# Kernel tuning notes

Hardware: AMD Instinct MI355X
Metric: run time of the kernel (lower is better)

Reference implementation:

```python
import jax, jax.numpy as jnp
import numpy as np

N = 50000
E = 1600000
IN_DIM = 256
HID = 128
EPS = 1e-5


def _bn(x, gamma, beta):
    # BatchNorm1d forward in training mode: biased batch stats
    mean = jnp.mean(x, axis=0)
    var = jnp.mean((x - mean) ** 2, axis=0)
    return (x - mean) * jax.lax.rsqrt(var + EPS) * gamma + beta


def _sage(x, edge_index, Wl, bl, Wr):
    # PyG SAGEConv with mean aggregation:
    #   out = lin_l(mean_{j in N(i)} x_j) + lin_r(x_i)
    src, dst = edge_index[0], edge_index[1]
    agg = jax.ops.segment_sum(x[src], dst, num_segments=N)          # [N, H]
    cnt = jax.ops.segment_sum(jnp.ones((src.shape[0],), x.dtype), dst, num_segments=N)
    mean = agg / jnp.maximum(cnt, 1.0)[:, None]
    return mean @ Wl + bl + x @ Wr


def setup_inputs() -> dict:
    key = jax.random.key(0)
    ks = jax.random.split(key, 16)
    s_in = 1.0 / np.sqrt(IN_DIM)
    s_h = 1.0 / np.sqrt(HID)
    return {
        "x": jax.random.normal(ks[0], (N, IN_DIM), jnp.float32),
        "edge_index": jax.random.randint(ks[1], (2, E), 0, N, jnp.int32),
        # input_linear: Linear(IN_DIM, HID) + BN
        "W_in": jax.random.uniform(ks[2], (IN_DIM, HID), jnp.float32, -s_in, s_in),
        "b_in": jax.random.uniform(ks[3], (HID,), jnp.float32, -s_in, s_in),
        "g1": jnp.ones((HID,), jnp.float32), "be1": jnp.zeros((HID,), jnp.float32),
        # hidden_linear: Linear(HID, HID) + BN
        "W_hid": jax.random.uniform(ks[4], (HID, HID), jnp.float32, -s_h, s_h),
        "b_hid": jax.random.uniform(ks[5], (HID,), jnp.float32, -s_h, s_h),
        "g2": jnp.ones((HID,), jnp.float32), "be2": jnp.zeros((HID,), jnp.float32),
        # graph_conv1: SAGEConv(HID, HID) + BN
        "Wl1": jax.random.uniform(ks[6], (HID, HID), jnp.float32, -s_h, s_h),
        "bl1": jax.random.uniform(ks[7], (HID,), jnp.float32, -s_h, s_h),
        "Wr1": jax.random.uniform(ks[8], (HID, HID), jnp.float32, -s_h, s_h),
        "g3": jnp.ones((HID,), jnp.float32), "be3": jnp.zeros((HID,), jnp.float32),
        # graph_conv2: SAGEConv(HID, HID) + BN
        "Wl2": jax.random.uniform(ks[9], (HID, HID), jnp.float32, -s_h, s_h),
        "bl2": jax.random.uniform(ks[10], (HID,), jnp.float32, -s_h, s_h),
        "Wr2": jax.random.uniform(ks[11], (HID, HID), jnp.float32, -s_h, s_h),
        "g4": jnp.ones((HID,), jnp.float32), "be4": jnp.zeros((HID,), jnp.float32),
    }


def reference(x, edge_index, W_in, b_in, g1, be1, W_hid, b_hid, g2, be2,
              Wl1, bl1, Wr1, g3, be3, Wl2, bl2, Wr2, g4, be4):
    feat = jax.nn.relu(_bn(x @ W_in + b_in, g1, be1))
    feat = jax.nn.relu(_bn(feat @ W_hid + b_hid, g2, be2))
    out = _bn(_sage(feat, edge_index, Wl1, bl1, Wr1), g3, be3)
    out = _bn(_sage(out, edge_index, Wl2, bl2, Wr2), g4, be4)
    return (feat, out)
```

## Files before the change

kernel.cpp:

```cpp
#include <hip/hip_runtime.h>
#include <stdint.h>

#define NN 50000
#define EE 1600000
#define IN_DIMC 256
#define HIDC 128
#define EPSC 1e-5f

#define NB 196
#define GA 512
#define CHUNK 3125

typedef unsigned short ushort_t;
typedef __attribute__((ext_vector_type(8))) short short8;
typedef __attribute__((ext_vector_type(4))) float floatx4;

static __device__ inline ushort_t f2bf(float f) {
    unsigned int u = __float_as_uint(f);
    u = u + 0x7fffu + ((u >> 16) & 1u);
    return (ushort_t)(u >> 16);
}
static __device__ inline unsigned int pack2(float a, float b) {
    return (unsigned int)f2bf(a) | ((unsigned int)f2bf(b) << 16);
}
static __device__ inline float bf2f(unsigned int bits16) {
    return __uint_as_float(bits16 << 16);
}

__global__ __launch_bounds__(256) void tcvt_all_kernel(
    const float* __restrict__ W_in, const float* __restrict__ W_hid,
    const float* __restrict__ Wl1, const float* __restrict__ Wr1,
    const float* __restrict__ Wl2, const float* __restrict__ Wr2,
    ushort_t* __restrict__ Wt_in, ushort_t* __restrict__ Wt_hid,
    ushort_t* __restrict__ Wtl1, ushort_t* __restrict__ Wtr1,
    ushort_t* __restrict__ Wtl2, ushort_t* __restrict__ Wtr2)
{
    const int idx = blockIdx.x * 256 + threadIdx.x;
    if (idx < 32768) {
        const int n = idx >> 8;
        const int k = idx & 255;
        Wt_in[idx] = f2bf(W_in[(size_t)k * 128 + n]);
    } else if (idx < 32768 + 5 * 16384) {
        const int r = idx - 32768;
        const int seg = r / 16384;
        const int j = r - seg * 16384;
        const int n = j >> 7;
        const int k = j & 127;
        const float* W; ushort_t* Wt;
        switch (seg) {
            case 0: W = W_hid; Wt = Wt_hid; break;
            case 1: W = Wl1;  Wt = Wtl1;  break;
            case 2: W = Wr1;  Wt = Wtr1;  break;
            case 3: W = Wl2;  Wt = Wtl2;  break;
            default: W = Wr2; Wt = Wtr2;  break;
        }
        Wt[j] = f2bf(W[(size_t)k * 128 + n]);
    }
}

__global__ __launch_bounds__(256) void mfma_gemm_kernel(
    const void* __restrict__ A1, const ushort_t* __restrict__ Wt1, int K1, int a1type,
    const void* __restrict__ A2, const ushort_t* __restrict__ Wt2, int K2,
    const float* __restrict__ bias, float* __restrict__ C, int M,
    const float* __restrict__ preStats, const float* __restrict__ preG,
    const float* __restrict__ preBe, float* __restrict__ outStats)
{
    __shared__ ushort_t As[64 * 72];
    __shared__ ushort_t Bs[128 * 72];
    __shared__ float aArr[128], bArr[128];
    __shared__ float red_s[4][64], red_q[4][64];

    const int t     = threadIdx.x;
    const int lane  = t & 63;
    const int wave  = t >> 6;
    const int quad  = lane >> 4;
    const int l15   = lane & 15;
    const int mhalf = wave & 1;
    const int nhalf = wave >> 1;
    const int row0  = blockIdx.x * 64;
    const int doAffine = (preStats != nullptr);

    if (doAffine && t < 128) {
        const float invM = 1.0f / (float)M;
        const float mean = preStats[t] * invM;
        float var = preStats[128 + t] * invM - mean * mean;
        if (var < 0.0f) var = 0.0f;
        const float s = preG[t] / sqrtf(var + EPSC);
        aArr[t] = s;
        bArr[t] = preBe[t] - mean * s;
    }
    if (doAffine) __syncthreads();

    floatx4 acc[2][4];
    #pragma unroll
    for (int i = 0; i < 2; i++)
        #pragma unroll
        for (int j = 0; j < 4; j++)
            acc[i][j] = (floatx4){0.0f, 0.0f, 0.0f, 0.0f};

    for (int s = 0; s < 2; s++) {
        const void*     A     = s ? A2  : A1;
        const ushort_t* Wt    = s ? Wt2 : Wt1;
        const int       K     = s ? K2  : K1;
        const int       atype = s ? 1   : a1type;
        if (A == nullptr) continue;

        for (int kc = 0; kc < K; kc += 64) {
            #pragma unroll
            for (int p = 0; p < 2; p++) {
                const int idx = p * 256 + t;
                const int r   = idx >> 3;
                const int c0  = (idx & 7) * 8;
                int gr = row0 + r;
                if (gr > M - 1) gr = M - 1;
                if (atype == 0) {
                    const float* Af = (const float*)A;
                    const size_t base = (size_t)gr * K + kc + c0;
                    float4 v0 = *(const float4*)(Af + base);
                    float4 v1 = *(const float4*)(Af + base + 4);
                    if (doAffine && s == 0) {
                        const int k0 = kc + c0;
                        v0.x = fmaxf(aArr[k0]     * v0.x + bArr[k0],     0.0f);
                        v0.y = fmaxf(aArr[k0 + 1] * v0.y + bArr[k0 + 1], 0.0f);
                        v0.z = fmaxf(aArr[k0 + 2] * v0.z + bArr[k0 + 2], 0.0f);
                        v0.w = fmaxf(aArr[k0 + 3] * v0.w + bArr[k0 + 3], 0.0f);
                        v1.x = fmaxf(aArr[k0 + 4] * v1.x + bArr[k0 + 4], 0.0f);
                        v1.y = fmaxf(aArr[k0 + 5] * v1.y + bArr[k0 + 5], 0.0f);
                        v1.z = fmaxf(aArr[k0 + 6] * v1.z + bArr[k0 + 6], 0.0f);
                        v1.w = fmaxf(aArr[k0 + 7] * v1.w + bArr[k0 + 7], 0.0f);
                    }
                    uint4 w;
                    w.x = pack2(v0.x, v0.y);
                    w.y = pack2(v0.z, v0.w);
                    w.z = pack2(v1.x, v1.y);
                    w.w = pack2(v1.z, v1.w);
                    *(uint4*)(As + r * 72 + c0) = w;
                } else {
                    const ushort_t* Ab = (const ushort_t*)A;
                    *(uint4*)(As + r * 72 + c0) =
                        *(const uint4*)(Ab + (size_t)gr * K + kc + c0);
                }
            }
            #pragma unroll
            for (int p = 0; p < 4; p++) {
                const int idx = p * 256 + t;
                const int n   = idx >> 3;
                const int c0  = (idx & 7) * 8;
                *(uint4*)(Bs + n * 72 + c0) =
                    *(const uint4*)(Wt + (size_t)n * K + kc + c0);
            }
            __syncthreads();

            #pragma unroll
            for (int ks = 0; ks < 2; ks++) {
                const int ko = ks * 32 + quad * 8;
                const short8 a0 = *(const short8*)(As + (mhalf * 32 + l15) * 72 + ko);
                const short8 a1 = *(const short8*)(As + (mhalf * 32 + 16 + l15) * 72 + ko);
                short8 b[4];
                #pragma unroll
                for (int j = 0; j < 4; j++)
                    b[j] = *(const short8*)(Bs + (nhalf * 64 + j * 16 + l15) * 72 + ko);
                #pragma unroll
                for (int j = 0; j < 4; j++) {
                    acc[0][j] = __builtin_amdgcn_mfma_f32_16x16x32_bf16(a0, b[j], acc[0][j], 0, 0, 0);
                    acc[1][j] = __builtin_amdgcn_mfma_f32_16x16x32_bf16(a1, b[j], acc[1][j], 0, 0, 0);
                }
            }
            __syncthreads();
        }
    }

    float s_[4], q_[4];
    #pragma unroll
    for (int j = 0; j < 4; j++) { s_[j] = 0.0f; q_[j] = 0.0f; }

    #pragma unroll
    for (int j = 0; j < 4; j++) {
        const int col = nhalf * 64 + j * 16 + l15;
        const float bv = bias[col];
        #pragma unroll
        for (int i = 0; i < 2; i++) {
            const int rbase = row0 + mhalf * 32 + i * 16 + quad * 4;
            #pragma unroll
            for (int reg = 0; reg < 4; reg++) {
                const float val = acc[i][j][reg] + bv;
                const int r_ = rbase + reg;
                if (r_ < M) {
                    C[(size_t)r_ * HIDC + col] = val;
                    s_[j] += val;
                    q_[j] += val * val;
                }
            }
        }
    }
    #pragma unroll
    for (int j = 0; j < 4; j++) {
        s_[j] += __shfl_xor(s_[j], 16, 64);
        s_[j] += __shfl_xor(s_[j], 32, 64);
        q_[j] += __shfl_xor(q_[j], 16, 64);
        q_[j] += __shfl_xor(q_[j], 32, 64);
    }
    if (quad == 0) {
        #pragma unroll
        for (int j = 0; j < 4; j++) {
            red_s[wave][j * 16 + l15] = s_[j];
            red_q[wave][j * 16 + l15] = q_[j];
        }
    }
    __syncthreads();
    if (t < 128) {
        const int c = t;
        const int g = c >> 6;
        const int cc = c & 63;
        const float S = red_s[g * 2][cc] + red_s[g * 2 + 1][cc];
        const float Q = red_q[g * 2][cc] + red_q[g * 2 + 1][cc];
        atomicAdd(&outStats[c], S);
        atomicAdd(&outStats[128 + c], Q);
    }
}

__global__ __launch_bounds__(256) void bn_apply_kernel(
    const float* __restrict__ src, float* __restrict__ dstF,
    ushort_t* __restrict__ dstB, const float* __restrict__ stats,
    const float* __restrict__ gamma, const float* __restrict__ beta,
    int relu, int M)
{
    __shared__ float sc[128], sh[128];
    const int t = threadIdx.x;
    if (t < 128) {
        const float invM = 1.0f / (float)M;
        const float mean = stats[t] * invM;
        float var = stats[128 + t] * invM - mean * mean;
        if (var < 0.0f) var = 0.0f;
        const float s = gamma[t] / sqrtf(var + EPSC);
        sc[t] = s;
        sh[t] = beta[t] - mean * s;
    }
    __syncthreads();

    const int total4 = M * HIDC / 4;
    for (int i = blockIdx.x * 256 + t; i < total4; i += gridDim.x * 256) {
        float4 v = ((const float4*)src)[i];
        const int c = (i * 4) & 127;
        v.x = v.x * sc[c]     + sh[c];
        v.y = v.y * sc[c + 1] + sh[c + 1];
        v.z = v.z * sc[c + 2] + sh[c + 2];
        v.w = v.w * sc[c + 3] + sh[c + 3];
        if (relu) {
            v.x = fmaxf(v.x, 0.0f); v.y = fmaxf(v.y, 0.0f);
            v.z = fmaxf(v.z, 0.0f); v.w = fmaxf(v.w, 0.0f);
        }
        if (dstF) ((float4*)dstF)[i] = v;
        if (dstB) {
            uint2 w;
            w.x = pack2(v.x, v.y);
            w.y = pack2(v.z, v.w);
            *(uint2*)(dstB + (size_t)i * 4) = w;
        }
    }
}

__global__ __launch_bounds__(256) void bucket_hist_kernel(
    const int* __restrict__ dstArr, int* __restrict__ hist2D)
{
    __shared__ int hist[NB];
    const int t = threadIdx.x;
    for (int i = t; i < NB; i += 256) hist[i] = 0;
    __syncthreads();
    const int e0 = blockIdx.x * CHUNK;
    const int e1 = e0 + CHUNK;
    for (int e = e0 + t; e < e1; e += 256)
        atomicAdd(&hist[dstArr[e] >> 8], 1);
    __syncthreads();
    for (int i = t; i < NB; i += 256)
        hist2D[(size_t)i * GA + blockIdx.x] = hist[i];
}

__global__ __launch_bounds__(256) void bucket_offsets_kernel(
    int* __restrict__ hist2D, int* __restrict__ bucketBase, int* __restrict__ rowp)
{
    __shared__ int wtot[4];
    const int t = threadIdx.x;
    int tot = 0;
    if (t < NB) {
        int4* p = (int4*)(hist2D + (size_t)t * GA);
        int s = 0;
        for (int i = 0; i < GA / 4; i++) {
            int4 h = p[i];
            int4 o;
            o.x = s; s += h.x;
            o.y = s; s += h.y;
            o.z = s; s += h.z;
            o.w = s; s += h.w;
            p[i] = o;
        }
        tot = s;
    }
    const int lane = t & 63, w = t >> 6;
    int x = tot;
    #pragma unroll
    for (int off = 1; off < 64; off <<= 1) {
        const int y = __shfl_up(x, off);
        if (lane >= off) x += y;
    }
    if (lane == 63) wtot[w] = x;
    __syncthreads();
    int woff = 0;
    #pragma unroll
    for (int j = 0; j < 4; j++) if (j < w) woff += wtot[j];
    const int excl = x + woff - tot;
    if (t < NB) bucketBase[t] = excl;
    if (t == 0) { bucketBase[NB] = EE; rowp[NN] = EE; }
}

__global__ __launch_bounds__(256) void bucket_scatter_kernel(
    const int* __restrict__ srcArr, const int* __restrict__ dstArr,
    const int* __restrict__ hist2D, const int* __restrict__ bucketBase,
    int2* __restrict__ ebuf)
{
    __shared__ int cur[NB];
    const int t = threadIdx.x;
    for (int i = t; i < NB; i += 256)
        cur[i] = bucketBase[i] + hist2D[(size_t)i * GA + blockIdx.x];
    __syncthreads();
    const int e0 = blockIdx.x * CHUNK;
    const int e1 = e0 + CHUNK;
    for (int e = e0 + t; e < e1; e += 256) {
        const int d = dstArr[e];
        const int s = srcArr[e];
        const int p = atomicAdd(&cur[d >> 8], 1);
        ebuf[p] = make_int2(s, d);
    }
}

__global__ __launch_bounds__(256) void fine_sort_kernel(
    const int2* __restrict__ ebuf, const int* __restrict__ bucketBase,
    int* __restrict__ rowp, int* __restrict__ col)
{
    __shared__ int cnt[256];
    __shared__ int wtot[4];
    const int b = blockIdx.x;
    const int t = threadIdx.x;
    const int bb0 = bucketBase[b];
    const int bb1 = bucketBase[b + 1];
    cnt[t] = 0;
    __syncthreads();
    for (int e = bb0 + t; e < bb1; e += 256)
        atomicAdd(&cnt[ebuf[e].y & 255], 1);
    __syncthreads();
    const int lane = t & 63, w = t >> 6;
    const int v = cnt[t];
    int x = v;
    #pragma unroll
    for (int off = 1; off < 64; off <<= 1) {
        const int y = __shfl_up(x, off);
        if (lane >= off) x += y;
    }
    if (lane == 63) wtot[w] = x;
    __syncthreads();
    int woff = 0;
    #pragma unroll
    for (int j = 0; j < 4; j++) if (j < w) woff += wtot[j];
    const int excl = x + woff - v;
    const int node = b * 256 + t;
    if (node < NN) rowp[node] = bb0 + excl;
    __syncthreads();
    cnt[t] = excl;
    __syncthreads();
    for (int e = bb0 + t; e < bb1; e += 256) {
        const int2 sd = ebuf[e];
        const int p = atomicAdd(&cnt[sd.y & 255], 1);
        col[bb0 + p] = sd.x;
    }
}

__global__ __launch_bounds__(256) void agg_kernel(
    const ushort_t* __restrict__ F, const int* __restrict__ row_ptr,
    const int* __restrict__ col, ushort_t* __restrict__ Mout)
{
    const int lane = threadIdx.x & 63;
    const int wave = blockIdx.x * (blockDim.x >> 6) + (threadIdx.x >> 6);
    const int nwaves = gridDim.x * (blockDim.x >> 6);
    const int coff = lane * 2;

    for (int n = wave; n < NN; n += nwaves) {
        const int b = __builtin_amdgcn_readfirstlane(row_ptr[n]);
        const int e = __builtin_amdgcn_readfirstlane(row_ptr[n + 1]);
        const int deg = e - b;
        float accx = 0.0f, accy = 0.0f;
        int j = b;
        for (; j + 8 <= e; j += 8) {
            const int s0 = col[j + 0];
            const int s1 = col[j + 1];
            const int s2 = col[j + 2];
            const int s3 = col[j + 3];
            const int s4 = col[j + 4];
            const int s5 = col[j + 5];
            const int s6 = col[j + 6];
            const int s7 = col[j + 7];
            const unsigned int v0 = *(const unsigned int*)(F + (size_t)s0 * HIDC + coff);
            const unsigned int v1 = *(const unsigned int*)(F + (size_t)s1 * HIDC + coff);
            const unsigned int v2 = *(const unsigned int*)(F + (size_t)s2 * HIDC + coff);
            const unsigned int v3 = *(const unsigned int*)(F + (size_t)s3 * HIDC + coff);
            const unsigned int v4 = *(const unsigned int*)(F + (size_t)s4 * HIDC + coff);
            const unsigned int v5 = *(const unsigned int*)(F + (size_t)s5 * HIDC + coff);
            const unsigned int v6 = *(const unsigned int*)(F + (size_t)s6 * HIDC + coff);
            const unsigned int v7 = *(const unsigned int*)(F + (size_t)s7 * HIDC + coff);
            accx += bf2f(v0 & 0xffffu) + bf2f(v1 & 0xffffu) + bf2f(v2 & 0xffffu)
                  + bf2f(v3 & 0xffffu) + bf2f(v4 & 0xffffu) + bf2f(v5 & 0xffffu)
                  + bf2f(v6 & 0xffffu) + bf2f(v7 & 0xffffu);
            accy += bf2f(v0 >> 16) + bf2f(v1 >> 16) + bf2f(v2 >> 16)
                  + bf2f(v3 >> 16) + bf2f(v4 >> 16) + bf2f(v5 >> 16)
                  + bf2f(v6 >> 16) + bf2f(v7 >> 16);
        }
        for (; j < e; j++) {
            const int s = col[j];
            const unsigned int v = *(const unsigned int*)(F + (size_t)s * HIDC + coff);
            accx += bf2f(v & 0xffffu);
            accy += bf2f(v >> 16);
        }
        const float inv = 1.0f / (float)(deg > 1 ? deg : 1);
        *(unsigned int*)(Mout + (size_t)n * HIDC + coff) =
            pack2(accx * inv, accy * inv);
    }
}

extern "C" void kernel_launch(void* const* d_in, const int* in_sizes, int n_in,
                              void* d_out, int out_size, void* d_ws, size_t ws_size,
                              hipStream_t stream)
{
    const float* x     = (const float*)d_in[0];
    const int*   ei    = (const int*)  d_in[1];
    const float* W_in  = (const float*)d_in[2];
    const float* b_in  = (const float*)d_in[3];
    const float* g1    = (const float*)d_in[4];
    const float* be1   = (const float*)d_in[5];
    const float* W_hid = (const float*)d_in[6];
    const float* b_hid = (const float*)d_in[7];
    const float* g2    = (const float*)d_in[8];
    const float* be2   = (const float*)d_in[9];
    const float* Wl1   = (const float*)d_in[10];
    const float* bl1   = (const float*)d_in[11];
    const float* Wr1   = (const float*)d_in[12];
    const float* g3    = (const float*)d_in[13];
    const float* be3   = (const float*)d_in[14];
    const float* Wl2   = (const float*)d_in[15];
    const float* bl2   = (const float*)d_in[16];
    const float* Wr2   = (const float*)d_in[17];
    const float* g4    = (const float*)d_in[18];
    const float* be4   = (const float*)d_in[19];

    const int* srcArr = ei;
    const int* dstArr = ei + EE;

    char* ws = (char*)d_ws;
    float*    bufA      = (float*)ws;    ws += (size_t)NN * HIDC * sizeof(float);
    float*    bufB      = (float*)ws;    ws += (size_t)NN * HIDC * sizeof(float);
    ushort_t* featB16   = (ushort_t*)ws; ws += (size_t)NN * HIDC * sizeof(ushort_t);
    ushort_t* o3B16     = (ushort_t*)ws; ws += (size_t)NN * HIDC * sizeof(ushort_t);
    ushort_t* aggB16    = (ushort_t*)ws; ws += (size_t)NN * HIDC * sizeof(ushort_t);
    float*    stats     = (float*)ws;    ws += 4 * 256 * sizeof(float);
    int*      hist2D    = (int*)ws;      ws += (size_t)NB * GA * sizeof(int);
    int*      bucketBase= (int*)ws;      ws += (NB + 4) * sizeof(int);
    int*      rowp      = (int*)ws;      ws += (size_t)(NN + 4) * sizeof(int);
    int*      colIdx    = (int*)ws;      ws += (size_t)EE * sizeof(int);
    int2*     ebuf      = (int2*)ws;     ws += (size_t)EE * sizeof(int2);
    ushort_t* Wt_in     = (ushort_t*)ws; ws += 128 * 256 * sizeof(ushort_t);
    ushort_t* Wt_hid    = (ushort_t*)ws; ws += 128 * 128 * sizeof(ushort_t);
    ushort_t* Wtl1      = (ushort_t*)ws; ws += 128 * 128 * sizeof(ushort_t);
    ushort_t* Wtr1      = (ushort_t*)ws; ws += 128 * 128 * sizeof(ushort_t);
    ushort_t* Wtl2      = (ushort_t*)ws; ws += 128 * 128 * sizeof(ushort_t);
    ushort_t* Wtr2      = (ushort_t*)ws; ws += 128 * 128 * sizeof(ushort_t);

    float* out0 = (float*)d_out;
    float* out1 = out0 + (size_t)NN * HIDC;

    hipMemsetAsync(stats, 0, 4 * 256 * sizeof(float), stream);

    tcvt_all_kernel<<<448, 256, 0, stream>>>(W_in, W_hid, Wl1, Wr1, Wl2, Wr2,
                                             Wt_in, Wt_hid, Wtl1, Wtr1, Wtl2, Wtr2);

    bucket_hist_kernel<<<GA, 256, 0, stream>>>(dstArr, hist2D);
    bucket_offsets_kernel<<<1, 256, 0, stream>>>(hist2D, bucketBase, rowp);
    bucket_scatter_kernel<<<GA, 256, 0, stream>>>(srcArr, dstArr, hist2D,
                                                  bucketBase, ebuf);
    fine_sort_kernel<<<NB, 256, 0, stream>>>(ebuf, bucketBase, rowp, colIdx);

    const int gemmGrid = (NN + 63) / 64;

    mfma_gemm_kernel<<<gemmGrid, 256, 0, stream>>>(
        x, Wt_in, IN_DIMC, 0, nullptr, nullptr, 0,
        b_in, bufA, NN, nullptr, nullptr, nullptr, stats + 0);

    mfma_gemm_kernel<<<gemmGrid, 256, 0, stream>>>(
        bufA, Wt_hid, HIDC, 0, nullptr, nullptr, 0,
        b_hid, bufB, NN, stats + 0, g1, be1, stats + 256);

    bn_apply_kernel<<<1024, 256, 0, stream>>>(bufB, out0, featB16,
                                              stats + 256, g2, be2, 1, NN);

    agg_kernel<<<4096, 256, 0, stream>>>(featB16, rowp, colIdx, aggB16);
    mfma_gemm_kernel<<<gemmGrid, 256, 0, stream>>>(
        aggB16, Wtl1, HIDC, 1, featB16, Wtr1, HIDC,
        bl1, bufA, NN, nullptr, nullptr, nullptr, stats + 512);

    bn_apply_kernel<<<1024, 256, 0, stream>>>(bufA, nullptr, o3B16,
                                              stats + 512, g3, be3, 0, NN);

    agg_kernel<<<4096, 256, 0, stream>>>(o3B16, rowp, colIdx, aggB16);
    mfma_gemm_kernel<<<gemmGrid, 256, 0, stream>>>(
        aggB16, Wtl2, HIDC, 1, o3B16, Wtr2, HIDC,
        bl2, bufB, NN, nullptr, nullptr, nullptr, stats + 768);

    bn_apply_kernel<<<1024, 256, 0, stream>>>(bufB, out1, nullptr,
                                              stats + 768, g4, be4, 0, NN);
}
```

Baseline: 475.1 us.

## Fuse neighbor aggregation into SAGE GEMM and fold BN into next layer weights

Replaces the separate aggregation kernel plus GEMM with a single kernel that gathers neighbor means directly into shared memory before the MFMA GEMM, removing the intermediate aggregated buffer. The third batch norm is folded into the second SAGE layer's weights and bias via a small fold kernel, eliminating one normalization pass. Edge sort buffer packs src/dst into one int to halve its traffic. Risks lower gather parallelism per block and bf16 storage of un-normalized activations.

```diff
diff --git a/kernel.cpp b/kernel.cpp
--- a/kernel.cpp
+++ b/kernel.cpp
@@ -30,17 +30,15 @@
 __global__ __launch_bounds__(256) void tcvt_all_kernel(
     const float* __restrict__ W_in, const float* __restrict__ W_hid,
     const float* __restrict__ Wl1, const float* __restrict__ Wr1,
-    const float* __restrict__ Wl2, const float* __restrict__ Wr2,
     ushort_t* __restrict__ Wt_in, ushort_t* __restrict__ Wt_hid,
-    ushort_t* __restrict__ Wtl1, ushort_t* __restrict__ Wtr1,
-    ushort_t* __restrict__ Wtl2, ushort_t* __restrict__ Wtr2)
+    ushort_t* __restrict__ Wtl1, ushort_t* __restrict__ Wtr1)
 {
     const int idx = blockIdx.x * 256 + threadIdx.x;
     if (idx < 32768) {
         const int n = idx >> 8;
         const int k = idx & 255;
         Wt_in[idx] = f2bf(W_in[(size_t)k * 128 + n]);
-    } else if (idx < 32768 + 5 * 16384) {
+    } else if (idx < 32768 + 3 * 16384) {
         const int r = idx - 32768;
         const int seg = r / 16384;
         const int j = r - seg * 16384;
@@ -50,17 +48,48 @@
         switch (seg) {
             case 0: W = W_hid; Wt = Wt_hid; break;
             case 1: W = Wl1;  Wt = Wtl1;  break;
-            case 2: W = Wr1;  Wt = Wtr1;  break;
-            case 3: W = Wl2;  Wt = Wtl2;  break;
-            default: W = Wr2; Wt = Wtr2;  break;
+            default: W = Wr1; Wt = Wtr1;  break;
         }
         Wt[j] = f2bf(W[(size_t)k * 128 + n]);
     }
 }
 
+__global__ __launch_bounds__(256) void fold_kernel(
+    const float* __restrict__ stats, const float* __restrict__ g,
+    const float* __restrict__ be, const float* __restrict__ Wl,
+    const float* __restrict__ Wr, const float* __restrict__ bl,
+    ushort_t* __restrict__ Wtlf, ushort_t* __restrict__ Wtrf,
+    float* __restrict__ bf)
+{
+    __shared__ float a[128], b[128];
+    const int t = threadIdx.x;
+    if (t < 128) {
+        const float invM = 1.0f / (float)NN;
+        const float mean = stats[t] * invM;
+        float var = stats[128 + t] * invM - mean * mean;
+        if (var < 0.0f) var = 0.0f;
+        const float s = g[t] / sqrtf(var + EPSC);
+        a[t] = s;
+        b[t] = be[t] - mean * s;
+    }
+    __syncthreads();
+    const int idx = blockIdx.x * 256 + t;
+    {
+        const int n = idx >> 7;
+        const int k = idx & 127;
+        Wtlf[idx] = f2bf(a[k] * Wl[(size_t)k * 128 + n]);
+        Wtrf[idx] = f2bf(a[k] * Wr[(size_t)k * 128 + n]);
+    }
+    if (blockIdx.x == 0 && t < 128) {
+        float s = bl[t];
+        for (int k = 0; k < 128; k++)
+            s += b[k] * (Wl[k * 128 + t] + Wr[k * 128 + t]);
+        bf[t] = s;
+    }
+}
+
 __global__ __launch_bounds__(256) void mfma_gemm_kernel(
-    const void* __restrict__ A1, const ushort_t* __restrict__ Wt1, int K1, int a1type,
-    const void* __restrict__ A2, const ushort_t* __restrict__ Wt2, int K2,
+    const float* __restrict__ A1, const ushort_t* __restrict__ Wt1, int K1,
     const float* __restrict__ bias, float* __restrict__ C, int M,
     const float* __restrict__ preStats, const float* __restrict__ preG,
     const float* __restrict__ preBe, float* __restrict__ outStats)
@@ -98,82 +127,67 @@
         for (int j = 0; j < 4; j++)
             acc[i][j] = (floatx4){0.0f, 0.0f, 0.0f, 0.0f};
 
-    for (int s = 0; s < 2; s++) {
-        const void*     A     = s ? A2  : A1;
-        const ushort_t* Wt    = s ? Wt2 : Wt1;
-        const int       K     = s ? K2  : K1;
-        const int       atype = s ? 1   : a1type;
-        if (A == nullptr) continue;
-
-        for (int kc = 0; kc < K; kc += 64) {
+    const int K = K1;
+    for (int kc = 0; kc < K; kc += 64) {
+        #pragma unroll
+        for (int p = 0; p < 2; p++) {
+            const int idx = p * 256 + t;
+            const int r   = idx >> 3;
+            const int c0  = (idx & 7) * 8;
+            int gr = row0 + r;
+            if (gr > M - 1) gr = M - 1;
+            const size_t base = (size_t)gr * K + kc + c0;
+            float4 v0 = *(const float4*)(A1 + base);
+            float4 v1 = *(const float4*)(A1 + base + 4);
+            if (doAffine) {
+                const int k0 = kc + c0;
+                v0.x = fmaxf(aArr[k0]     * v0.x + bArr[k0],     0.0f);
+                v0.y = fmaxf(aArr[k0 + 1] * v0.y + bArr[k0 + 1], 0.0f);
+                v0.z = fmaxf(aArr[k0 + 2] * v0.z + bArr[k0 + 2], 0.0f);
+                v0.w = fmaxf(aArr[k0 + 3] * v0.w + bArr[k0 + 3], 0.0f);
+                v1.x = fmaxf(aArr[k0 + 4] * v1.x + bArr[k0 + 4], 0.0f);
+                v1.y = fmaxf(aArr[k0 + 5] * v1.y + bArr[k0 + 5], 0.0f);
+                v1.z = fmaxf(aArr[k0 + 6] * v1.z + bArr[k0 + 6], 0.0f);
+                v1.w = fmaxf(aArr[k0 + 7] * v1.w + bArr[k0 + 7], 0.0f);
+            }
+            uint4 w;
+            w.x = pack2(v0.x, v0.y);
+            w.y = pack2(v0.z, v0.w);
+            w.z = pack2(v1.x, v1.y);
+            w.w = pack2(v1.z, v1.w);
+            *(uint4*)(As + r * 72 + c0) = w;
+        }
+        #pragma unroll
+        for (int p = 0; p < 4; p++) {
+            const int idx = p * 256 + t;
+            const int n   = idx >> 3;
+            const int c0  = (idx & 7) * 8;
+            *(uint4*)(Bs + n * 72 + c0) =
+                *(const uint4*)(Wt1 + (size_t)n * K + kc + c0);
+        }
+        __syncthreads();
+
+        #pragma unroll
+        for (int ks = 0; ks < 2; ks++) {
+            const int ko = ks * 32 + quad * 8;
+            const short8 a0 = *(const short8*)(As + (mhalf * 32 + l15) * 72 + ko);
+            const short8 a1 = *(const short8*)(As + (mhalf * 32 + 16 + l15) * 72 + ko);
+            short8 b[4];
             #pragma unroll
-            for (int p = 0; p < 2; p++) {
-                const int idx = p * 256 + t;
-                const int r   = idx >> 3;
-                const int c0  = (idx & 7) * 8;
-                int gr = row0 + r;
-                if (gr > M - 1) gr = M - 1;
-                if (atype == 0) {
-                    const float* Af = (const float*)A;
-                    const size_t base = (size_t)gr * K + kc + c0;
-                    float4 v0 = *(const float4*)(Af + base);
-                    float4 v1 = *(const float4*)(Af + base + 4);
-                    if (doAffine && s == 0) {
-                        const int k0 = kc + c0;
-                        v0.x = fmaxf(aArr[k0]     * v0.x + bArr[k0],     0.0f);
-                        v0.y = fmaxf(aArr[k0 + 1] * v0.y + bArr[k0 + 1], 0.0f);
-                        v0.z = fmaxf(aArr[k0 + 2] * v0.z + bArr[k0 + 2], 0.0f);
-                        v0.w = fmaxf(aArr[k0 + 3] * v0.w + bArr[k0 + 3], 0.0f);
-                        v1.x = fmaxf(aArr[k0 + 4] * v1.x + bArr[k0 + 4], 0.0f);
-                        v1.y = fmaxf(aArr[k0 + 5] * v1.y + bArr[k0 + 5], 0.0f);
-                        v1.z = fmaxf(aArr[k0 + 6] * v1.z + bArr[k0 + 6], 0.0f);
-                        v1.w = fmaxf(aArr[k0 + 7] * v1.w + bArr[k0 + 7], 0.0f);
-                    }
-                    uint4 w;
-                    w.x = pack2(v0.x, v0.y);
-                    w.y = pack2(v0.z, v0.w);
-                    w.z = pack2(v1.x, v1.y);
-                    w.w = pack2(v1.z, v1.w);
-                    *(uint4*)(As + r * 72 + c0) = w;
-                } else {
-                    const ushort_t* Ab = (const ushort_t*)A;
-                    *(uint4*)(As + r * 72 + c0) =
-                        *(const uint4*)(Ab + (size_t)gr * K + kc + c0);
-                }
+            for (int j = 0; j < 4; j++)
+                b[j] = *(const short8*)(Bs + (nhalf * 64 + j * 16 + l15) * 72 + ko);
+            #pragma unroll
+            for (int j = 0; j < 4; j++) {
+                acc[0][j] = __builtin_amdgcn_mfma_f32_16x16x32_bf16(a0, b[j], acc[0][j], 0, 0, 0);
+                acc[1][j] = __builtin_amdgcn_mfma_f32_16x16x32_bf16(a1, b[j], acc[1][j], 0, 0, 0);
             }
-            #pragma unroll
-            for (int p = 0; p < 4; p++) {
-                const int idx = p * 256 + t;
-                const int n   = idx >> 3;
-                const int c0  = (idx & 7) * 8;
-                *(uint4*)(Bs + n * 72 + c0) =
-                    *(const uint4*)(Wt + (size_t)n * K + kc + c0);
-            }
-            __syncthreads();
-
-            #pragma unroll
-            for (int ks = 0; ks < 2; ks++) {
-                const int ko = ks * 32 + quad * 8;
-                const short8 a0 = *(const short8*)(As + (mhalf * 32 + l15) * 72 + ko);
-                const short8 a1 = *(const short8*)(As + (mhalf * 32 + 16 + l15) * 72 + ko);
-                short8 b[4];
-                #pragma unroll
-                for (int j = 0; j < 4; j++)
-                    b[j] = *(const short8*)(Bs + (nhalf * 64 + j * 16 + l15) * 72 + ko);
-                #pragma unroll
-                for (int j = 0; j < 4; j++) {
-                    acc[0][j] = __builtin_amdgcn_mfma_f32_16x16x32_bf16(a0, b[j], acc[0][j], 0, 0, 0);
-                    acc[1][j] = __builtin_amdgcn_mfma_f32_16x16x32_bf16(a1, b[j], acc[1][j], 0, 0, 0);
-                }
-            }
-            __syncthreads();
-        }
+        }
+        __syncthreads();
     }
 
     float s_[4], q_[4];
     #pragma unroll
     for (int j = 0; j < 4; j++) { s_[j] = 0.0f; q_[j] = 0.0f; }
-
     #pragma unroll
     for (int j = 0; j < 4; j++) {
         const int col = nhalf * 64 + j * 16 + l15;
@@ -209,13 +223,174 @@
     }
     __syncthreads();
     if (t < 128) {
-        const int c = t;
-        const int g = c >> 6;
-        const int cc = c & 63;
-        const float S = red_s[g * 2][cc] + red_s[g * 2 + 1][cc];
-        const float Q = red_q[g * 2][cc] + red_q[g * 2 + 1][cc];
-        atomicAdd(&outStats[c], S);
-        atomicAdd(&outStats[128 + c], Q);
+        const int g = t >> 6;
+        const int cc = t & 63;
+        atomicAdd(&outStats[t],       red_s[g * 2][cc] + red_s[g * 2 + 1][cc]);
+        atomicAdd(&outStats[128 + t], red_q[g * 2][cc] + red_q[g * 2 + 1][cc]);
+    }
+}
+
+__global__ __launch_bounds__(256) void sage_gemm_kernel(
+    const ushort_t* __restrict__ F,
+    const int* __restrict__ rowp, const int* __restrict__ colIdx,
+    const ushort_t* __restrict__ Wtl, const ushort_t* __restrict__ Wtr,
+    const float* __restrict__ bias,
+    float* __restrict__ Cf, ushort_t* __restrict__ Cb,
+    float* __restrict__ outStats)
+{
+    __shared__ ushort_t AsG[2 * 64 * 72];
+    __shared__ ushort_t Bs[128 * 72];
+    __shared__ float red_s[4][64], red_q[4][64];
+
+    const int t     = threadIdx.x;
+    const int lane  = t & 63;
+    const int wave  = t >> 6;
+    const int quad  = lane >> 4;
+    const int l15   = lane & 15;
+    const int mhalf = wave & 1;
+    const int nhalf = wave >> 1;
+    const int row0  = blockIdx.x * 64;
+
+    const int coff   = lane * 2;
+    const int chunk  = lane >> 5;
+    const int klocal = (lane * 2) & 63;
+    for (int i = 0; i < 16; i++) {
+        const int r = wave * 16 + i;
+        int gn = row0 + r; if (gn > NN - 1) gn = NN - 1;
+        const int b = __builtin_amdgcn_readfirstlane(rowp[gn]);
+        const int e = __builtin_amdgcn_readfirstlane(rowp[gn + 1]);
+        float ax = 0.0f, ay = 0.0f;
+        int j = b;
+        for (; j + 8 <= e; j += 8) {
+            const int s0 = colIdx[j + 0];
+            const int s1 = colIdx[j + 1];
+            const int s2 = colIdx[j + 2];
+            const int s3 = colIdx[j + 3];
+            const int s4 = colIdx[j + 4];
+            const int s5 = colIdx[j + 5];
+            const int s6 = colIdx[j + 6];
+            const int s7 = colIdx[j + 7];
+            const unsigned int v0 = *(const unsigned int*)(F + (size_t)s0 * HIDC + coff);
+            const unsigned int v1 = *(const unsigned int*)(F + (size_t)s1 * HIDC + coff);
+            const unsigned int v2 = *(const unsigned int*)(F + (size_t)s2 * HIDC + coff);
+            const unsigned int v3 = *(const unsigned int*)(F + (size_t)s3 * HIDC + coff);
+            const unsigned int v4 = *(const unsigned int*)(F + (size_t)s4 * HIDC + coff);
+            const unsigned int v5 = *(const unsigned int*)(F + (size_t)s5 * HIDC + coff);
+            const unsigned int v6 = *(const unsigned int*)(F + (size_t)s6 * HIDC + coff);
+            const unsigned int v7 = *(const unsigned int*)(F + (size_t)s7 * HIDC + coff);
+            ax += bf2f(v0 & 0xffffu) + bf2f(v1 & 0xffffu) + bf2f(v2 & 0xffffu)
+                + bf2f(v3 & 0xffffu) + bf2f(v4 & 0xffffu) + bf2f(v5 & 0xffffu)
+                + bf2f(v6 & 0xffffu) + bf2f(v7 & 0xffffu);
+            ay += bf2f(v0 >> 16) + bf2f(v1 >> 16) + bf2f(v2 >> 16)
+                + bf2f(v3 >> 16) + bf2f(v4 >> 16) + bf2f(v5 >> 16)
+                + bf2f(v6 >> 16) + bf2f(v7 >> 16);
+        }
+        for (; j < e; j++) {
+            const int s = colIdx[j];
+            const unsigned int v = *(const unsigned int*)(F + (size_t)s * HIDC + coff);
+            ax += bf2f(v & 0xffffu);
+            ay += bf2f(v >> 16);
+        }
+        const int dg = e - b;
+        const float inv = 1.0f / (float)(dg > 1 ? dg : 1);
+        *(unsigned int*)(AsG + chunk * 4608 + r * 72 + klocal) = pack2(ax * inv, ay * inv);
+    }
+    __syncthreads();
+
+    floatx4 acc[2][4];
+    #pragma unroll
+    for (int i = 0; i < 2; i++)
+        #pragma unroll
+        for (int j = 0; j < 4; j++)
+            acc[i][j] = (floatx4){0.0f, 0.0f, 0.0f, 0.0f};
+
+    for (int s = 0; s < 2; s++) {
+        const ushort_t* Wt = s ? Wtr : Wtl;
+        for (int kcI = 0; kcI < 2; kcI++) {
+            if (s == 1) {
+                #pragma unroll
+                for (int p = 0; p < 2; p++) {
+                    const int idx = p * 256 + t;
+                    const int r  = idx >> 3;
+                    const int c0 = (idx & 7) * 8;
+                    int gr = row0 + r; if (gr > NN - 1) gr = NN - 1;
+                    *(uint4*)(AsG + r * 72 + c0) =
+                        *(const uint4*)(F + (size_t)gr * HIDC + kcI * 64 + c0);
+                }
+            }
+            #pragma unroll
+            for (int p = 0; p < 4; p++) {
+                const int idx = p * 256 + t;
+                const int n  = idx >> 3;
+                const int c0 = (idx & 7) * 8;
+                *(uint4*)(Bs + n * 72 + c0) =
+                    *(const uint4*)(Wt + (size_t)n * HIDC + kcI * 64 + c0);
+            }
+            __syncthreads();
+
+            const ushort_t* Ab = (s == 0) ? (AsG + kcI * 4608) : AsG;
+            #pragma unroll
+            for (int ks = 0; ks < 2; ks++) {
+                const int ko = ks * 32 + quad * 8;
+                const short8 a0 = *(const short8*)(Ab + (mhalf * 32 + l15) * 72 + ko);
+                const short8 a1 = *(const short8*)(Ab + (mhalf * 32 + 16 + l15) * 72 + ko);
+                short8 b[4];
+                #pragma unroll
+                for (int j = 0; j < 4; j++)
+                    b[j] = *(const short8*)(Bs + (nhalf * 64 + j * 16 + l15) * 72 + ko);
+                #pragma unroll
+                for (int j = 0; j < 4; j++) {
+                    acc[0][j] = __builtin_amdgcn_mfma_f32_16x16x32_bf16(a0, b[j], acc[0][j], 0, 0, 0);
+                    acc[1][j] = __builtin_amdgcn_mfma_f32_16x16x32_bf16(a1, b[j], acc[1][j], 0, 0, 0);
+                }
+            }
+            __syncthreads();
+        }
+    }
+
+    float s_[4], q_[4];
+    #pragma unroll
+    for (int j = 0; j < 4; j++) { s_[j] = 0.0f; q_[j] = 0.0f; }
+    #pragma unroll
+    for (int j = 0; j < 4; j++) {
+        const int col = nhalf * 64 + j * 16 + l15;
+        const float bv = bias[col];
+        #pragma unroll
+        for (int i = 0; i < 2; i++) {
+            const int rbase = row0 + mhalf * 32 + i * 16 + quad * 4;
+            #pragma unroll
+            for (int reg = 0; reg < 4; reg++) {
+                const float val = acc[i][j][reg] + bv;
+                const int r_ = rbase + reg;
+                if (r_ < NN) {
+                    if (Cf) Cf[(size_t)r_ * HIDC + col] = val;
+                    if (Cb) Cb[(size_t)r_ * HIDC + col] = f2bf(val);
+                    s_[j] += val;
+                    q_[j] += val * val;
+                }
+            }
+        }
+    }
+    #pragma unroll
+    for (int j = 0; j < 4; j++) {
+        s_[j] += __shfl_xor(s_[j], 16, 64);
+        s_[j] += __shfl_xor(s_[j], 32, 64);
+        q_[j] += __shfl_xor(q_[j], 16, 64);
+        q_[j] += __shfl_xor(q_[j], 32, 64);
+    }
+    if (quad == 0) {
+        #pragma unroll
+        for (int j = 0; j < 4; j++) {
+            red_s[wave][j * 16 + l15] = s_[j];
+            red_q[wave][j * 16 + l15] = q_[j];
+        }
+    }
+    __syncthreads();
+    if (t < 128) {
+        const int g = t >> 6;
+        const int cc = t & 63;
+        atomicAdd(&outStats[t],       red_s[g * 2][cc] + red_s[g * 2 + 1][cc]);
+        atomicAdd(&outStats[128 + t], red_q[g * 2][cc] + red_q[g * 2 + 1][cc]);
     }
 }
 
@@ -316,7 +491,7 @@
 __global__ __launch_bounds__(256) void bucket_scatter_kernel(
     const int* __restrict__ srcArr, const int* __restrict__ dstArr,
     const int* __restrict__ hist2D, const int* __restrict__ bucketBase,
-    int2* __restrict__ ebuf)
+    int* __restrict__ ebuf)
 {
     __shared__ int cur[NB];
     const int t = threadIdx.x;
@@ -329,12 +504,12 @@
         const int d = dstArr[e];
         const int s = srcArr[e];
         const int p = atomicAdd(&cur[d >> 8], 1);
-        ebuf[p] = make_int2(s, d);
+        ebuf[p] = (s << 8) | (d & 255);
     }
 }
 
 __global__ __launch_bounds__(256) void fine_sort_kernel(
-    const int2* __restrict__ ebuf, const int* __restrict__ bucketBase,
+    const int* __restrict__ ebuf, const int* __restrict__ bucketBase,
     int* __restrict__ rowp, int* __restrict__ col)
 {
     __shared__ int cnt[256];
@@ -346,7 +521,7 @@
     cnt[t] = 0;
     __syncthreads();
     for (int e = bb0 + t; e < bb1; e += 256)
-        atomicAdd(&cnt[ebuf[e].y & 255], 1);
+        atomicAdd(&cnt[ebuf[e] & 255], 1);
     __syncthreads();
     const int lane = t & 63, w = t >> 6;
     const int v = cnt[t];
@@ -368,60 +543,9 @@
     cnt[t] = excl;
     __syncthreads();
     for (int e = bb0 + t; e < bb1; e += 256) {
-        const int2 sd = ebuf[e];
-        const int p = atomicAdd(&cnt[sd.y & 255], 1);
-        col[bb0 + p] = sd.x;
-    }
-}
-
-__global__ __launch_bounds__(256) void agg_kernel(
-    const ushort_t* __restrict__ F, const int* __restrict__ row_ptr,
-    const int* __restrict__ col, ushort_t* __restrict__ Mout)
-{
-    const int lane = threadIdx.x & 63;
-    const int wave = blockIdx.x * (blockDim.x >> 6) + (threadIdx.x >> 6);
-    const int nwaves = gridDim.x * (blockDim.x >> 6);
-    const int coff = lane * 2;
-
-    for (int n = wave; n < NN; n += nwaves) {
-        const int b = __builtin_amdgcn_readfirstlane(row_ptr[n]);
-        const int e = __builtin_amdgcn_readfirstlane(row_ptr[n + 1]);
-        const int deg = e - b;
-        float accx = 0.0f, accy = 0.0f;
-        int j = b;
-        for (; j + 8 <= e; j += 8) {
-            const int s0 = col[j + 0];
-            const int s1 = col[j + 1];
-            const int s2 = col[j + 2];
-            const int s3 = col[j + 3];
-            const int s4 = col[j + 4];
-            const int s5 = col[j + 5];
-            const int s6 = col[j + 6];
-            const int s7 = col[j + 7];
-            const unsigned int v0 = *(const unsigned int*)(F + (size_t)s0 * HIDC + coff);
-            const unsigned int v1 = *(const unsigned int*)(F + (size_t)s1 * HIDC + coff);
-            const unsigned int v2 = *(const unsigned int*)(F + (size_t)s2 * HIDC + coff);
-            const unsigned int v3 = *(const unsigned int*)(F + (size_t)s3 * HIDC + coff);
-            const unsigned int v4 = *(const unsigned int*)(F + (size_t)s4 * HIDC + coff);
-            const unsigned int v5 = *(const unsigned int*)(F + (size_t)s5 * HIDC + coff);
-            const unsigned int v6 = *(const unsigned int*)(F + (size_t)s6 * HIDC + coff);
-            const unsigned int v7 = *(const unsigned int*)(F + (size_t)s7 * HIDC + coff);
-            accx += bf2f(v0 & 0xffffu) + bf2f(v1 & 0xffffu) + bf2f(v2 & 0xffffu)
-                  + bf2f(v3 & 0xffffu) + bf2f(v4 & 0xffffu) + bf2f(v5 & 0xffffu)
-                  + bf2f(v6 & 0xffffu) + bf2f(v7 & 0xffffu);
-            accy += bf2f(v0 >> 16) + bf2f(v1 >> 16) + bf2f(v2 >> 16)
-                  + bf2f(v3 >> 16) + bf2f(v4 >> 16) + bf2f(v5 >> 16)
-                  + bf2f(v6 >> 16) + bf2f(v7 >> 16);
-        }
-        for (; j < e; j++) {
-            const int s = col[j];
-            const unsigned int v = *(const unsigned int*)(F + (size_t)s * HIDC + coff);
-            accx += bf2f(v & 0xffffu);
-            accy += bf2f(v >> 16);
-        }
-        const float inv = 1.0f / (float)(deg > 1 ? deg : 1);
-        *(unsigned int*)(Mout + (size_t)n * HIDC + coff) =
-            pack2(accx * inv, accy * inv);
+        const int sd = ebuf[e];
+        const int p = atomicAdd(&cnt[sd & 255], 1);
+        col[bb0 + p] = (unsigned)sd >> 8;
     }
 }
 
@@ -458,27 +582,27 @@
     float*    bufB      = (float*)ws;    ws += (size_t)NN * HIDC * sizeof(float);
     ushort_t* featB16   = (ushort_t*)ws; ws += (size_t)NN * HIDC * sizeof(ushort_t);
     ushort_t* o3B16     = (ushort_t*)ws; ws += (size_t)NN * HIDC * sizeof(ushort_t);
-    ushort_t* aggB16    = (ushort_t*)ws; ws += (size_t)NN * HIDC * sizeof(ushort_t);
     float*    stats     = (float*)ws;    ws += 4 * 256 * sizeof(float);
     int*      hist2D    = (int*)ws;      ws += (size_t)NB * GA * sizeof(int);
     int*      bucketBase= (int*)ws;      ws += (NB + 4) * sizeof(int);
     int*      rowp      = (int*)ws;      ws += (size_t)(NN + 4) * sizeof(int);
     int*      colIdx    = (int*)ws;      ws += (size_t)EE * sizeof(int);
-    int2*     ebuf      = (int2*)ws;     ws += (size_t)EE * sizeof(int2);
+    int*      ebuf      = (int*)ws;      ws += (size_t)EE * sizeof(int);
     ushort_t* Wt_in     = (ushort_t*)ws; ws += 128 * 256 * sizeof(ushort_t);
     ushort_t* Wt_hid    = (ushort_t*)ws; ws += 128 * 128 * sizeof(ushort_t);
     ushort_t* Wtl1      = (ushort_t*)ws; ws += 128 * 128 * sizeof(ushort_t);
     ushort_t* Wtr1      = (ushort_t*)ws; ws += 128 * 128 * sizeof(ushort_t);
-    ushort_t* Wtl2      = (ushort_t*)ws; ws += 128 * 128 * sizeof(ushort_t);
-    ushort_t* Wtr2      = (ushort_t*)ws; ws += 128 * 128 * sizeof(ushort_t);
+    ushort_t* Wtl2f     = (ushort_t*)ws; ws += 128 * 128 * sizeof(ushort_t);
+    ushort_t* Wtr2f     = (ushort_t*)ws; ws += 128 * 128 * sizeof(ushort_t);
+    float*    bf2       = (float*)ws;    ws += 128 * sizeof(float);
 
     float* out0 = (float*)d_out;
     float* out1 = out0 + (size_t)NN * HIDC;
 
     hipMemsetAsync(stats, 0, 4 * 256 * sizeof(float), stream);
 
-    tcvt_all_kernel<<<448, 256, 0, stream>>>(W_in, W_hid, Wl1, Wr1, Wl2, Wr2,
-                                             Wt_in, Wt_hid, Wtl1, Wtr1, Wtl2, Wtr2);
+    tcvt_all_kernel<<<320, 256, 0, stream>>>(W_in, W_hid, Wl1, Wr1,
+                                             Wt_in, Wt_hid, Wtl1, Wtr1);
 
     bucket_hist_kernel<<<GA, 256, 0, stream>>>(dstArr, hist2D);
     bucket_offsets_kernel<<<1, 256, 0, stream>>>(hist2D, bucketBase, rowp);
@@ -489,28 +613,26 @@
     const int gemmGrid = (NN + 63) / 64;
 
     mfma_gemm_kernel<<<gemmGrid, 256, 0, stream>>>(
-        x, Wt_in, IN_DIMC, 0, nullptr, nullptr, 0,
-        b_in, bufA, NN, nullptr, nullptr, nullptr, stats + 0);
+        x, Wt_in, IN_DIMC, b_in, bufA, NN,
+        nullptr, nullptr, nullptr, stats + 0);
 
     mfma_gemm_kernel<<<gemmGrid, 256, 0, stream>>>(
-        bufA, Wt_hid, HIDC, 0, nullptr, nullptr, 0,
-        b_hid, bufB, NN, stats + 0, g1, be1, stats + 256);
+        bufA, Wt_hid, HIDC, b_hid, bufB, NN,
+        stats + 0, g1, be1, stats + 256);
 
     bn_apply_kernel<<<1024, 256, 0, stream>>>(bufB, out0, featB16,
                                               stats + 256, g2, be2, 1, NN);
 
-    agg_kernel<<<4096, 256, 0, stream>>>(featB16, rowp, colIdx, aggB16);
-    mfma_gemm_kernel<<<gemmGrid, 256, 0, stream>>>(
-        aggB16, Wtl1, HIDC, 1, featB16, Wtr1, HIDC,
-        bl1, bufA, NN, nullptr, nullptr, nullptr, stats + 512);
-
-    bn_apply_kernel<<<1024, 256, 0, stream>>>(bufA, nullptr, o3B16,
-                                              stats + 512, g3, be3, 0, NN);
-
-    agg_kernel<<<4096, 256, 0, stream>>>(o3B16, rowp, colIdx, aggB16);
-    mfma_gemm_kernel<<<gemmGrid, 256, 0, stream>>>(
-        aggB16, Wtl2, HIDC, 1, o3B16, Wtr2, HIDC,
-        bl2, bufB, NN, nullptr, nullptr, nullptr, stats + 768);
+    sage_gemm_kernel<<<gemmGrid, 256, 0, stream>>>(
+        featB16, rowp, colIdx, Wtl1, Wtr1, bl1,
+        nullptr, o3B16, stats + 512);
+
+    fold_kernel<<<64, 256, 0, stream>>>(stats + 512, g3, be3, Wl2, Wr2, bl2,
+                                        Wtl2f, Wtr2f, bf2);
+
+    sage_gemm_kernel<<<gemmGrid, 256, 0, stream>>>(
+        o3B16, rowp, colIdx, Wtl2f, Wtr2f, bf2,
+        bufB, nullptr, stats + 768);
 
     bn_apply_kernel<<<1024, 256, 0, stream>>>(bufB, out1, nullptr,
                                               stats + 768, g4, be4, 0, NN);
```

Measured after the change: 488.2 us. 2.8% more time.
